# Optimization experiments

Hardware: AMD Instinct MI355X
Metric: run time of the kernel (lower is better)

Reference implementation:

```python
import jax, jax.numpy as jnp
import numpy as np

B, N, D_FEAT = 16, 4096, 64
NPOINT, NSAMPLE = 1024, 32
MLP = [64, 64, 128]
IN_CH = 3 + D_FEAT
EPS = 1e-5  # BatchNorm eps (torch default)


def _fps(xyz, npoint):
    # Farthest point sampling; sequential scan over npoint steps (matches torch loop).
    b, n, _ = xyz.shape
    def step(carry, _):
        distance, farthest = carry  # (B,N) running min dist, (B,) current centroid idx
        centroid = jnp.take_along_axis(xyz, farthest[:, None, None], axis=1)  # (B,1,3)
        d = jnp.sum((xyz - centroid) ** 2, -1)  # (B,N)
        distance = jnp.minimum(distance, d)
        nxt = jnp.argmax(distance, -1).astype(jnp.int32)
        return (distance, nxt), farthest
    init = (jnp.full((b, n), jnp.inf, dtype=xyz.dtype),
            jnp.full((b,), n // 2, dtype=jnp.int32))
    _, centroids = jax.lax.scan(step, init, None, length=npoint)
    return centroids.T  # (B, npoint)


def _gather(pts, idx):
    # pts: (B,N,C); idx: (B,...) int -> (B,...,C)
    return jax.vmap(lambda p, i: p[i])(pts, idx)


def setup_inputs() -> dict:
    key = jax.random.key(0)
    ks = jax.random.split(key, 16)
    inp = {
        'xyz': jax.random.normal(ks[0], (B, N, 3), jnp.float32),
        'points': jax.random.normal(ks[1], (B, N, D_FEAT), jnp.float32),
    }
    last = IN_CH
    for li, oc in enumerate(MLP):
        inp[f'W{li}'] = jax.random.normal(ks[2 + li], (oc, last), jnp.float32) * (1.0 / np.sqrt(last))
        inp[f'b{li}'] = jnp.zeros((oc,), jnp.float32)
        inp[f'g{li}'] = jnp.ones((oc,), jnp.float32)
        inp[f'be{li}'] = jnp.zeros((oc,), jnp.float32)
        last = oc
    C = MLP[-1]; R = C // 8
    inp['aW1'] = jax.random.normal(ks[10], (R, C), jnp.float32) * (1.0 / np.sqrt(C))
    inp['aW2'] = jax.random.normal(ks[11], (C, R), jnp.float32) * (1.0 / np.sqrt(R))
    return inp


def reference(xyz, points, W0, b0, g0, be0, W1, b1, g1, be1, W2, b2, g2, be2, aW1, aW2):
    fps_idx = _fps(xyz, NPOINT)                 # (B,S) int32
    new_xyz = _gather(xyz, fps_idx)             # (B,S,3)
    # squared distances (B,S,N) via matmul expansion (as torch square_distance)
    d = (-2.0 * jnp.einsum('bsc,bnc->bsn', new_xyz, xyz)
         + jnp.sum(new_xyz ** 2, -1)[..., None]
         + jnp.sum(xyz ** 2, -1)[:, None, :])
    _, idx = jax.lax.top_k(-d, NSAMPLE)         # (B,S,k) nearest neighbors
    grouped_xyz = _gather(xyz, idx)             # (B,S,k,3)
    rel = grouped_xyz - new_xyz[:, :, None, :]  # relative coords
    feat = _gather(points, idx)                 # (B,S,k,D)
    g = jnp.concatenate([rel, feat], axis=-1)   # (B,S,k,3+D) channels-last
    # 1x1 conv MLP + BatchNorm (training-mode batch stats) + ReLU
    for (W, b, ga, be) in ((W0, b0, g0, be0), (W1, b1, g1, be1), (W2, b2, g2, be2)):
        g = jnp.einsum('bskc,oc->bsko', g, W) + b
        mu = g.mean(axis=(0, 1, 2))
        var = g.var(axis=(0, 1, 2))
        g = ga * (g - mu) * jax.lax.rsqrt(var + EPS) + be
        g = jax.nn.relu(g)
    new_points = g.max(axis=2)                  # max over nsample -> (B,S,C)
    # channel attention on (B,C,S) == reductions over S here
    avg = new_points.mean(axis=1)               # (B,C)
    mx = new_points.max(axis=1)                 # (B,C)
    def fc(v):
        return jnp.einsum('cr,br->bc', aW2, jax.nn.relu(jnp.einsum('rc,bc->br', aW1, v)))
    scale = jax.nn.sigmoid(fc(avg) + fc(mx))    # (B,C)
    new_points = new_points * scale[:, None, :]
    return new_xyz, new_points, fps_idx
```

## Files before the change

### kernel.cpp

```cpp
#include <hip/hip_runtime.h>
#include <hip/hip_bf16.h>

#define BB 16
#define NN 4096
#define SS 1024
#define KS 32
#define DF 64
#define INC 67
#define C1 64
#define C2 64
#define C3 128
#define ROWS (BB*SS*KS)
#define EPSBN 1e-5f
#define F_INF (__builtin_inff())

typedef __bf16 bf16;
typedef __bf16 bfrag __attribute__((ext_vector_type(8)));
typedef float  ffrag __attribute__((ext_vector_type(4)));
typedef float  f2    __attribute__((ext_vector_type(2)));
typedef unsigned long long u64;

#define OUT_NXYZ 0
#define OUT_NP   49152
#define OUT_FPS  2146304

#define OFF_FPS   0u
#define OFF_NXYZ  65536u
#define OFF_IDX   262144u
#define OFF_STATS 2359296u
#define OFF_ASUM  2555904u
#define OFF_AMAX  2621440u
#define OFF_BNC   2686976u
#define OFF_SCALE 2690048u
#define OFF_NP0   2698240u
#define OFF_YMAX  11086848u
#define OFF_H1    19475456u
#define OFF_H2    86584320u
#define ZERO_BYTES (196608u + 65536u + 65536u)

#define DPP_MAX_STEP(k, ctrl, rmask, bc) { \
  int _lo = __builtin_amdgcn_update_dpp(0, (int)(unsigned)(k), (ctrl), (rmask), 0xf, (bc)); \
  int _hi = __builtin_amdgcn_update_dpp(0, (int)((k)>>32),     (ctrl), (rmask), 0xf, (bc)); \
  u64 _k2 = ((u64)(unsigned)_hi << 32) | (unsigned)_lo; \
  if (_k2 > (k)) (k) = _k2; }

__device__ __forceinline__ u64 dpp_wavemax64(u64 k){
  DPP_MAX_STEP(k, 0x111, 0xf, true)
  DPP_MAX_STEP(k, 0x112, 0xf, true)
  DPP_MAX_STEP(k, 0x114, 0xf, true)
  DPP_MAX_STEP(k, 0x118, 0xf, true)
  DPP_MAX_STEP(k, 0x142, 0xa, false)
  DPP_MAX_STEP(k, 0x143, 0xc, false)
  return k;
}

__global__ __launch_bounds__(256) void fps_kernel(const float* __restrict__ xyz,
                                                  int* __restrict__ fps_i,
                                                  float* __restrict__ nxyz_ws,
                                                  float* __restrict__ out)
{
  #pragma clang fp contract(off)
  __shared__ __align__(16) float4 lc[NN];
  __shared__ int lfps[SS];
  __shared__ u64 slotk[2][4];
  int b = blockIdx.x, t = threadIdx.x;
  const float* xb = xyz + (size_t)b*NN*3;
  for (int p = t; p < NN; p += 256){
    lc[p] = make_float4(xb[p*3], xb[p*3+1], xb[p*3+2], 0.f);
  }
  __syncthreads();
  f2 px2[8], py2[8], pz2[8], pd2[8];
  int p0 = t*16;
  #pragma unroll
  for (int j=0;j<8;++j){
    float4 a = lc[p0+2*j], c = lc[p0+2*j+1];
    px2[j] = (f2){a.x, c.x}; py2[j] = (f2){a.y, c.y}; pz2[j] = (f2){a.z, c.z};
    pd2[j] = (f2){F_INF, F_INF};
  }
  float cx = lc[NN/2].x, cy = lc[NN/2].y, cz = lc[NN/2].z;
  if (t==0) lfps[0]=NN/2;
  int wv = t >> 6, lane = t & 63;
  for (int it=1; it<SS; ++it){
    f2 c2x = (f2){cx,cx}, c2y = (f2){cy,cy}, c2z = (f2){cz,cz};
    float bv=-1.f; int bi=p0;
    #pragma unroll
    for (int j=0;j<8;++j){
      f2 dx = px2[j]-c2x, dy = py2[j]-c2y, dz = pz2[j]-c2z;
      f2 d = (dx*dx + dy*dy) + dz*dz;
      f2 nd = (f2){fminf(pd2[j].x, d.x), fminf(pd2[j].y, d.y)};
      pd2[j]=nd;
      if (nd.x > bv){ bv=nd.x; bi=p0+2*j; }
      if (nd.y > bv){ bv=nd.y; bi=p0+2*j+1; }
    }
    u64 key = ((u64)__float_as_uint(bv) << 32) | (unsigned)(~bi);
    key = dpp_wavemax64(key);
    key = __shfl(key, 63);
    int p = it & 1;
    if (lane == 0) slotk[p][wv] = key;
    __syncthreads();
    u64 k = slotk[p][t & 3];
    DPP_MAX_STEP(k, 0xB1, 0xf, true)
    DPP_MAX_STEP(k, 0x4E, 0xf, true)
    int i = ~(unsigned)k;
    float4 cc = lc[i];
    cx = cc.x; cy = cc.y; cz = cc.z;
    if (t==0) lfps[it]=i;
  }
  __syncthreads();
  for (int s=t; s<SS; s+=256){
    int i = lfps[s];
    fps_i[b*SS+s]=i;
    out[OUT_FPS + b*SS + s] = (float)i;
    float4 cc = lc[i];
    int o3 = (b*SS+s)*3;
    out[OUT_NXYZ+o3]=cc.x; out[OUT_NXYZ+o3+1]=cc.y; out[OUT_NXYZ+o3+2]=cc.z;
    nxyz_ws[o3]=cc.x; nxyz_ws[o3+1]=cc.y; nxyz_ws[o3+2]=cc.z;
  }
}

__global__ __launch_bounds__(64) void knn_kernel(const float* __restrict__ xyz,
                                                 const float* __restrict__ nxyz,
                                                 int* __restrict__ knn)
{
  __shared__ float ld[NN];
  int lane = threadIdx.x;
  int bs = blockIdx.x;
  int b = bs >> 10;
  const float* xb = xyz + (size_t)b*NN*3;
  float sx=nxyz[bs*3], sy=nxyz[bs*3+1], sz=nxyz[bs*3+2];
  float gv[8]; int gi[8];
  float lv = F_INF; int li = 0;
  #pragma unroll
  for (int g=0; g<8; ++g){
    float bgv = F_INF; int bgi = 0;
    #pragma unroll
    for (int jj=0; jj<8; ++jj){
      int p = (g*8+jj)*64 + lane;
      float dx=xb[p*3]-sx, dy=xb[p*3+1]-sy, dz=xb[p*3+2]-sz;
      float d = dx*dx+dy*dy+dz*dz;
      ld[p] = d;
      if (d < bgv){ bgv=d; bgi=p; }
    }
    gv[g]=bgv; gi[g]=bgi;
    if (bgv < lv){ lv=bgv; li=bgi; }
  }
  int kept = 0;
  for (int it=0; it<KS; ++it){
    u64 mk = ~(((u64)__float_as_uint(lv) << 32) | (unsigned)li);
    mk = dpp_wavemax64(mk);
    mk = __shfl(mk, 63);
    int i = (int)(unsigned)(~mk);
    if (lane==it) kept = i;
    if ((i & 63) == lane){
      int j = i >> 6;
      ld[i] = F_INF;
      int g = j >> 3;
      float bgv=F_INF; int bgi=0;
      for (int jj=0;jj<8;++jj){
        int p = (g*8+jj)*64 + lane;
        float d = ld[p];
        if (d<bgv){bgv=d;bgi=p;}
      }
      #pragma unroll
      for (int q=0;q<8;++q){ if (q==g){ gv[q]=bgv; gi[q]=bgi; } }
      lv=F_INF; li=0;
      #pragma unroll
      for (int q=0;q<8;++q){ if (gv[q]<lv){ lv=gv[q]; li=gi[q]; } }
    }
  }
  if (lane < KS) knn[bs*KS + lane] = kept;
}

__global__ __launch_bounds__(256) void conv1_kernel(const float* __restrict__ xyz,
                                                    const float* __restrict__ points,
                                                    const float* __restrict__ W0,
                                                    const float* __restrict__ b0,
                                                    const float* __restrict__ nxyz,
                                                    const int* __restrict__ knn,
                                                    bf16* __restrict__ h1,
                                                    float* __restrict__ stats)
{
  __shared__ __align__(16) bf16 As[64][104];
  __shared__ __align__(16) bf16 Bs[64][104];
  __shared__ float s1[C1], s2[C1];
  int t = threadIdx.x;
  int Rbase = blockIdx.x * 64;
  if (t < C1){ s1[t]=0.f; s2[t]=0.f; }
  {
    int o = t >> 2, q = t & 3;
    const float* wr = W0 + o*INC;
    for (int cc = q*24; cc < q*24+24; ++cc){
      float w;
      if (cc < 64) w = wr[3+cc];
      else if (cc < 67) w = wr[cc-64];
      else w = 0.f;
      Bs[o][cc] = (bf16)w;
    }
  }
  {
    int r = t >> 2, q = t & 3;
    int R = Rbase + r;
    int bs = R >> 5;
    int bIdx = bs >> 10;
    int nI = knn[R];
    const float* pr = points + ((size_t)(bIdx*NN + nI))*DF + q*16;
    float4 f0 = *(const float4*)(pr);
    float4 f1 = *(const float4*)(pr+4);
    float4 f2v = *(const float4*)(pr+8);
    float4 f3 = *(const float4*)(pr+12);
    bf16* ap = &As[r][q*16];
    ap[0]=(bf16)f0.x; ap[1]=(bf16)f0.y; ap[2]=(bf16)f0.z; ap[3]=(bf16)f0.w;
    ap[4]=(bf16)f1.x; ap[5]=(bf16)f1.y; ap[6]=(bf16)f1.z; ap[7]=(bf16)f1.w;
    ap[8]=(bf16)f2v.x; ap[9]=(bf16)f2v.y; ap[10]=(bf16)f2v.z; ap[11]=(bf16)f2v.w;
    ap[12]=(bf16)f3.x; ap[13]=(bf16)f3.y; ap[14]=(bf16)f3.z; ap[15]=(bf16)f3.w;
    if (q==0){
      const float* xr = xyz + ((size_t)(bIdx*NN + nI))*3;
      const float* nr = nxyz + bs*3;
      As[r][64]=(bf16)(xr[0]-nr[0]);
      As[r][65]=(bf16)(xr[1]-nr[1]);
      As[r][66]=(bf16)(xr[2]-nr[2]);
      for (int cc=67; cc<96; ++cc) As[r][cc]=(bf16)0.f;
    }
  }
  __syncthreads();
  int wv = t >> 6, lane = t & 63;
  int row16 = wv * 16;
  int arow = lane & 15, kgrp = lane >> 4;
  ffrag acc[4] = {};
  #pragma unroll
  for (int kc = 0; kc < 3; ++kc){
    bfrag af = *(const bfrag*)&As[row16 + arow][kc*32 + kgrp*8];
    #pragma unroll
    for (int nt = 0; nt < 4; ++nt){
      bfrag bfv = *(const bfrag*)&Bs[nt*16 + arow][kc*32 + kgrp*8];
      acc[nt] = __builtin_amdgcn_mfma_f32_16x16x32_bf16(af, bfv, acc[nt], 0,0,0);
    }
  }
  #pragma unroll
  for (int nt=0; nt<4; ++nt){
    int c = nt*16 + arow;
    float bias = b0[c];
    float ls1=0.f, ls2=0.f;
    #pragma unroll
    for (int r=0;r<4;++r){
      float y = acc[nt][r] + bias;
      int grow = Rbase + row16 + kgrp*4 + r;
      h1[(size_t)grow*C1 + c] = (bf16)y;
      ls1 += y; ls2 += y*y;
    }
    ls1 += __shfl_xor(ls1, 16); ls1 += __shfl_xor(ls1, 32);
    ls2 += __shfl_xor(ls2, 16); ls2 += __shfl_xor(ls2, 32);
    if (kgrp==0){ atomicAdd(&s1[c], ls1); atomicAdd(&s2[c], ls2); }
  }
  __syncthreads();
  if (t < C1){
    float* gp = stats + (blockIdx.x & 63)*256;
    atomicAdd(&gp[t], s1[t]);
    atomicAdd(&gp[128 + t], s2[t]);
  }
}

__global__ void bnfin_kernel(const float* __restrict__ stats, const float* __restrict__ g,
                             const float* __restrict__ be, float* __restrict__ bnc, int C)
{
  int c = threadIdx.x; if (c >= C) return;
  float a1=0.f, a2=0.f;
  for (int q=0;q<64;++q){ a1 += stats[q*256+c]; a2 += stats[q*256+128+c]; }
  float inv = 1.f/(float)ROWS;
  float mu = a1*inv; float var = a2*inv - mu*mu;
  float a = g[c]*rsqrtf(var + EPSBN);
  bnc[c] = a; bnc[128+c] = be[c] - mu*a;
}

__global__ __launch_bounds__(256) void conv2_kernel(const bf16* __restrict__ h1,
                                                    const float* __restrict__ W1,
                                                    const float* __restrict__ b1,
                                                    const float* __restrict__ bnc,
                                                    bf16* __restrict__ h2,
                                                    float* __restrict__ stats)
{
  __shared__ __align__(16) bf16 As[64][72];
  __shared__ __align__(16) bf16 Bs[64][72];
  __shared__ float s1[C2], s2[C2];
  int t = threadIdx.x;
  int Rbase = blockIdx.x * 64;
  if (t < C2){ s1[t]=0.f; s2[t]=0.f; }
  {
    int o = t >> 2, q = t & 3;
    const float* wr = W1 + o*64 + q*16;
    bf16* bp = &Bs[o][q*16];
    #pragma unroll
    for (int v=0; v<4; ++v){
      float4 f = *(const float4*)(wr + v*4);
      bp[v*4+0]=(bf16)f.x; bp[v*4+1]=(bf16)f.y; bp[v*4+2]=(bf16)f.z; bp[v*4+3]=(bf16)f.w;
    }
  }
  {
    int r = t >> 2, q = t & 3;
    int R = Rbase + r;
    const bf16* hr = h1 + (size_t)R*64 + q*16;
    bfrag h0 = *(const bfrag*)hr;
    bfrag h1v = *(const bfrag*)(hr+8);
    #pragma unroll
    for (int j=0;j<8;++j){
      int c=q*16+j;
      As[r][c] = (bf16)fmaxf(fmaf(bnc[c], (float)h0[j], bnc[128+c]), 0.f);
    }
    #pragma unroll
    for (int j=0;j<8;++j){
      int c=q*16+8+j;
      As[r][c] = (bf16)fmaxf(fmaf(bnc[c], (float)h1v[j], bnc[128+c]), 0.f);
    }
  }
  __syncthreads();
  int wv = t >> 6, lane = t & 63;
  int row16 = wv * 16;
  int arow = lane & 15, kgrp = lane >> 4;
  ffrag acc[4] = {};
  #pragma unroll
  for (int kc = 0; kc < 2; ++kc){
    bfrag af = *(const bfrag*)&As[row16 + arow][kc*32 + kgrp*8];
    #pragma unroll
    for (int nt = 0; nt < 4; ++nt){
      bfrag bfv = *(const bfrag*)&Bs[nt*16 + arow][kc*32 + kgrp*8];
      acc[nt] = __builtin_amdgcn_mfma_f32_16x16x32_bf16(af, bfv, acc[nt], 0,0,0);
    }
  }
  #pragma unroll
  for (int nt=0; nt<4; ++nt){
    int c = nt*16 + arow;
    float bias = b1[c];
    float ls1=0.f, ls2=0.f;
    #pragma unroll
    for (int r=0;r<4;++r){
      float y = acc[nt][r] + bias;
      int grow = Rbase + row16 + kgrp*4 + r;
      h2[(size_t)grow*C2 + c] = (bf16)y;
      ls1 += y; ls2 += y*y;
    }
    ls1 += __shfl_xor(ls1, 16); ls1 += __shfl_xor(ls1, 32);
    ls2 += __shfl_xor(ls2, 16); ls2 += __shfl_xor(ls2, 32);
    if (kgrp==0){ atomicAdd(&s1[c], ls1); atomicAdd(&s2[c], ls2); }
  }
  __syncthreads();
  if (t < C2){
    float* gp = stats + (blockIdx.x & 63)*256;
    atomicAdd(&gp[t], s1[t]);
    atomicAdd(&gp[128 + t], s2[t]);
  }
}

__global__ __launch_bounds__(256) void conv3_kernel(const bf16* __restrict__ h2,
                                                    const float* __restrict__ W2,
                                                    const float* __restrict__ b2,
                                                    const float* __restrict__ bnc,
                                                    float* __restrict__ ymax,
                                                    float* __restrict__ stats)
{
  __shared__ __align__(16) bf16 As[64][72];
  __shared__ __align__(16) bf16 Bs[128][72];
  __shared__ float s1[C3], s2[C3];
  __shared__ float wmax[4][C3];
  int t = threadIdx.x;
  int Rbase = blockIdx.x * 64;
  if (t < C3){ s1[t]=0.f; s2[t]=0.f; }
  {
    int o = t >> 1, q = t & 1;
    const float* wr = W2 + o*64 + q*32;
    bf16* bp = &Bs[o][q*32];
    #pragma unroll
    for (int v=0; v<8; ++v){
      float4 f = *(const float4*)(wr + v*4);
      bp[v*4+0]=(bf16)f.x; bp[v*4+1]=(bf16)f.y; bp[v*4+2]=(bf16)f.z; bp[v*4+3]=(bf16)f.w;
    }
  }
  {
    int r = t >> 2, q = t & 3;
    int R = Rbase + r;
    const bf16* hr = h2 + (size_t)R*64 + q*16;
    bfrag h0 = *(const bfrag*)hr;
    bfrag h1v = *(const bfrag*)(hr+8);
    #pragma unroll
    for (int j=0;j<8;++j){
      int c=q*16+j;
      As[r][c] = (bf16)fmaxf(fmaf(bnc[c], (float)h0[j], bnc[128+c]), 0.f);
    }
    #pragma unroll
    for (int j=0;j<8;++j){
      int c=q*16+8+j;
      As[r][c] = (bf16)fmaxf(fmaf(bnc[c], (float)h1v[j], bnc[128+c]), 0.f);
    }
  }
  __syncthreads();
  int wv = t >> 6, lane = t & 63;
  int row16 = wv * 16;
  int arow = lane & 15, kgrp = lane >> 4;
  ffrag acc[8] = {};
  #pragma unroll
  for (int kc = 0; kc < 2; ++kc){
    bfrag af = *(const bfrag*)&As[row16 + arow][kc*32 + kgrp*8];
    #pragma unroll
    for (int nt = 0; nt < 8; ++nt){
      bfrag bfv = *(const bfrag*)&Bs[nt*16 + arow][kc*32 + kgrp*8];
      acc[nt] = __builtin_amdgcn_mfma_f32_16x16x32_bf16(af, bfv, acc[nt], 0,0,0);
    }
  }
  #pragma unroll
  for (int nt=0; nt<8; ++nt){
    int c = nt*16 + arow;
    float bias = b2[c];
    float ls1=0.f, ls2=0.f, mm=-F_INF;
    #pragma unroll
    for (int r=0;r<4;++r){
      float y = acc[nt][r] + bias;
      ls1 += y; ls2 += y*y; mm = fmaxf(mm, y);
    }
    ls1 += __shfl_xor(ls1, 16); ls1 += __shfl_xor(ls1, 32);
    ls2 += __shfl_xor(ls2, 16); ls2 += __shfl_xor(ls2, 32);
    mm = fmaxf(mm, __shfl_xor(mm, 16)); mm = fmaxf(mm, __shfl_xor(mm, 32));
    if (kgrp==0){ atomicAdd(&s1[c], ls1); atomicAdd(&s2[c], ls2); wmax[wv][c]=mm; }
  }
  __syncthreads();
  {
    int half = t >> 7;
    int c = t & 127;
    float m = fmaxf(wmax[half*2][c], wmax[half*2+1][c]);
    ymax[(size_t)(blockIdx.x*2 + half)*C3 + c] = m;
  }
  if (t < C3){
    float* gp = stats + (blockIdx.x & 63)*256;
    atomicAdd(&gp[t], s1[t]);
    atomicAdd(&gp[128 + t], s2[t]);
  }
}

__global__ __launch_bounds__(256) void attreduce_kernel(const float* __restrict__ ymax,
                                                        const float* __restrict__ bnc,
                                                        float* __restrict__ np0,
                                                        float* __restrict__ asum,
                                                        unsigned* __restrict__ amax)
{
  __shared__ float rs[256], rm[256];
  int t = threadIdx.x;
  int b = blockIdx.x >> 3, sg = blockIdx.x & 7;
  int c = t & 127, h = t >> 7;
  float a = bnc[c], bb = bnc[128+c];
  size_t base = ((size_t)(b*1024 + sg*128 + h*64))*128 + c;
  float s = 0.f, m = 0.f;
  #pragma unroll 4
  for (int j=0;j<64;++j){
    float v = fmaxf(fmaf(a, ymax[base + (size_t)j*128], bb), 0.f);
    np0[base + (size_t)j*128] = v;
    s += v; m = fmaxf(m, v);
  }
  rs[t]=s; rm[t]=m;
  __syncthreads();
  if (t < 128){
    float s2 = rs[t] + rs[t+128];
    float m2 = fmaxf(rm[t], rm[t+128]);
    atomicAdd(&asum[b*128+t], s2);
    atomicMax(&amax[b*128+t], __float_as_uint(m2));
  }
}

__global__ __launch_bounds__(256) void attn_kernel(const float* __restrict__ asum,
                                                   const unsigned* __restrict__ amax,
                                                   const float* __restrict__ aW1,
                                                   const float* __restrict__ aW2,
                                                   float* __restrict__ scale)
{
  __shared__ float avg[16][128], mx[16][128], hA[16][16], hM[16][16];
  int t = threadIdx.x;
  for (int i=t; i<2048; i+=256){
    int b=i>>7, c=i&127;
    avg[b][c]=asum[i]*(1.f/1024.f); mx[b][c]=__uint_as_float(amax[i]);
  }
  __syncthreads();
  {
    int b=t>>4, r=t&15;
    float sa=0.f, sm=0.f;
    for (int c=0;c<128;++c){ float w=aW1[r*128+c]; sa+=w*avg[b][c]; sm+=w*mx[b][c]; }
    hA[b][r]=fmaxf(sa,0.f); hM[b][r]=fmaxf(sm,0.f);
  }
  __syncthreads();
  for (int i=t;i<2048;i+=256){
    int b=i>>7,c=i&127;
    float o=0.f;
    for (int r=0;r<16;++r){ o += aW2[c*16+r]*(hA[b][r]+hM[b][r]); }
    scale[i] = 1.f/(1.f+expf(-o));
  }
}

__global__ __launch_bounds__(256) void finout_kernel(const float* __restrict__ np0,
                                                     const float* __restrict__ scale,
                                                     float* __restrict__ out)
{
  int i = blockIdx.x*256 + threadIdx.x;
  int c = i & 127; int b = i >> 17;
  out[OUT_NP + i] = np0[i] * scale[b*128+c];
}

extern "C" void kernel_launch(void* const* d_in, const int* in_sizes, int n_in,
                              void* d_out, int out_size, void* d_ws, size_t ws_size,
                              hipStream_t stream)
{
  const float* xyz    = (const float*)d_in[0];
  const float* points = (const float*)d_in[1];
  const float* W0 = (const float*)d_in[2];
  const float* b0 = (const float*)d_in[3];
  const float* g0 = (const float*)d_in[4];
  const float* be0= (const float*)d_in[5];
  const float* W1 = (const float*)d_in[6];
  const float* b1 = (const float*)d_in[7];
  const float* g1 = (const float*)d_in[8];
  const float* be1= (const float*)d_in[9];
  const float* W2 = (const float*)d_in[10];
  const float* b2 = (const float*)d_in[11];
  const float* g2 = (const float*)d_in[12];
  const float* be2= (const float*)d_in[13];
  const float* aW1= (const float*)d_in[14];
  const float* aW2= (const float*)d_in[15];
  float* out = (float*)d_out;
  char* ws = (char*)d_ws;

  int*      fpsI  = (int*)(ws + OFF_FPS);
  float*    nxyz  = (float*)(ws + OFF_NXYZ);
  int*      knnI  = (int*)(ws + OFF_IDX);
  float*    stats = (float*)(ws + OFF_STATS);
  float*    asum  = (float*)(ws + OFF_ASUM);
  unsigned* amax  = (unsigned*)(ws + OFF_AMAX);
  float*    bnc   = (float*)(ws + OFF_BNC);
  float*    scl   = (float*)(ws + OFF_SCALE);
  float*    np0   = (float*)(ws + OFF_NP0);
  float*    ymax  = (float*)(ws + OFF_YMAX);
  bf16*     h1    = (bf16*)(ws + OFF_H1);
  bf16*     h2    = (bf16*)(ws + OFF_H2);

  hipMemsetAsync(ws + OFF_STATS, 0, ZERO_BYTES, stream);
  fps_kernel<<<BB, 256, 0, stream>>>(xyz, fpsI, nxyz, out);
  knn_kernel<<<BB*SS, 64, 0, stream>>>(xyz, nxyz, knnI);
  conv1_kernel<<<ROWS/64, 256, 0, stream>>>(xyz, points, W0, b0, nxyz, knnI, h1, stats);
  bnfin_kernel<<<1, 128, 0, stream>>>(stats, g0, be0, bnc, C1);
  conv2_kernel<<<ROWS/64, 256, 0, stream>>>(h1, W1, b1, bnc, h2, stats + 64*256);
  bnfin_kernel<<<1, 128, 0, stream>>>(stats + 64*256, g1, be1, bnc + 256, C2);
  conv3_kernel<<<ROWS/64, 256, 0, stream>>>(h2, W2, b2, bnc + 256, ymax, stats + 2*64*256);
  bnfin_kernel<<<1, 128, 0, stream>>>(stats + 2*64*256, g2, be2, bnc + 512, C3);
  attreduce_kernel<<<BB*8, 256, 0, stream>>>(ymax, bnc + 512, np0, asum, amax);
  attn_kernel<<<1, 256, 0, stream>>>(asum, amax, aW1, aW2, scl);
  finout_kernel<<<(BB*SS*C3)/256, 256, 0, stream>>>(np0, scl, out);
}
```

Before: 1.087 ms.

## Widen FPS to 512 threads, SoA coords, readlane broadcast for wave max

The farthest-point-sampling kernel now runs 512 threads per batch with 8 points per thread. This halves the serial per-iteration distance work but adds two more waves to the per-step block barrier and the cross-wave reduction. Coordinates move from float4 AoS to separate x/y/z shared arrays. The lane-63 broadcast after the DPP wave max switches from a shuffle to scalar readlane in both the FPS and KNN kernels, to shorten the latency-bound reduction chain.

```diff
diff --git a/kernel.cpp b/kernel.cpp
--- a/kernel.cpp
+++ b/kernel.cpp
@@ -54,37 +54,42 @@
   return k;
 }
 
-__global__ __launch_bounds__(256) void fps_kernel(const float* __restrict__ xyz,
+__device__ __forceinline__ u64 bcast63(u64 k){
+  unsigned lo = (unsigned)__builtin_amdgcn_readlane((int)(unsigned)k, 63);
+  unsigned hi = (unsigned)__builtin_amdgcn_readlane((int)(k>>32), 63);
+  return ((u64)hi<<32) | lo;
+}
+
+__global__ __launch_bounds__(512) void fps_kernel(const float* __restrict__ xyz,
                                                   int* __restrict__ fps_i,
                                                   float* __restrict__ nxyz_ws,
                                                   float* __restrict__ out)
 {
   #pragma clang fp contract(off)
-  __shared__ __align__(16) float4 lc[NN];
+  __shared__ float lx[NN], ly[NN], lz[NN];
   __shared__ int lfps[SS];
-  __shared__ u64 slotk[2][4];
+  __shared__ u64 slotk[2][8];
   int b = blockIdx.x, t = threadIdx.x;
   const float* xb = xyz + (size_t)b*NN*3;
-  for (int p = t; p < NN; p += 256){
-    lc[p] = make_float4(xb[p*3], xb[p*3+1], xb[p*3+2], 0.f);
-  }
-  __syncthreads();
-  f2 px2[8], py2[8], pz2[8], pd2[8];
-  int p0 = t*16;
-  #pragma unroll
-  for (int j=0;j<8;++j){
-    float4 a = lc[p0+2*j], c = lc[p0+2*j+1];
-    px2[j] = (f2){a.x, c.x}; py2[j] = (f2){a.y, c.y}; pz2[j] = (f2){a.z, c.z};
+  for (int p = t; p < NN; p += 512){ lx[p]=xb[p*3]; ly[p]=xb[p*3+1]; lz[p]=xb[p*3+2]; }
+  __syncthreads();
+  f2 px2[4], py2[4], pz2[4], pd2[4];
+  int p0 = t*8;
+  #pragma unroll
+  for (int j=0;j<4;++j){
+    px2[j] = (f2){lx[p0+2*j], lx[p0+2*j+1]};
+    py2[j] = (f2){ly[p0+2*j], ly[p0+2*j+1]};
+    pz2[j] = (f2){lz[p0+2*j], lz[p0+2*j+1]};
     pd2[j] = (f2){F_INF, F_INF};
   }
-  float cx = lc[NN/2].x, cy = lc[NN/2].y, cz = lc[NN/2].z;
+  float cx = lx[NN/2], cy = ly[NN/2], cz = lz[NN/2];
   if (t==0) lfps[0]=NN/2;
   int wv = t >> 6, lane = t & 63;
   for (int it=1; it<SS; ++it){
     f2 c2x = (f2){cx,cx}, c2y = (f2){cy,cy}, c2z = (f2){cz,cz};
     float bv=-1.f; int bi=p0;
     #pragma unroll
-    for (int j=0;j<8;++j){
+    for (int j=0;j<4;++j){
       f2 dx = px2[j]-c2x, dy = py2[j]-c2y, dz = pz2[j]-c2z;
       f2 d = (dx*dx + dy*dy) + dz*dz;
       f2 nd = (f2){fminf(pd2[j].x, d.x), fminf(pd2[j].y, d.y)};
@@ -94,27 +99,27 @@
     }
     u64 key = ((u64)__float_as_uint(bv) << 32) | (unsigned)(~bi);
     key = dpp_wavemax64(key);
-    key = __shfl(key, 63);
+    key = bcast63(key);
     int p = it & 1;
     if (lane == 0) slotk[p][wv] = key;
     __syncthreads();
-    u64 k = slotk[p][t & 3];
+    u64 k = slotk[p][t & 7];
     DPP_MAX_STEP(k, 0xB1, 0xf, true)
     DPP_MAX_STEP(k, 0x4E, 0xf, true)
+    DPP_MAX_STEP(k, 0x141, 0xf, true)
     int i = ~(unsigned)k;
-    float4 cc = lc[i];
-    cx = cc.x; cy = cc.y; cz = cc.z;
+    cx = lx[i]; cy = ly[i]; cz = lz[i];
     if (t==0) lfps[it]=i;
   }
   __syncthreads();
-  for (int s=t; s<SS; s+=256){
+  for (int s=t; s<SS; s+=512){
     int i = lfps[s];
     fps_i[b*SS+s]=i;
     out[OUT_FPS + b*SS + s] = (float)i;
-    float4 cc = lc[i];
+    float xx=lx[i], yy=ly[i], zz=lz[i];
     int o3 = (b*SS+s)*3;
-    out[OUT_NXYZ+o3]=cc.x; out[OUT_NXYZ+o3+1]=cc.y; out[OUT_NXYZ+o3+2]=cc.z;
-    nxyz_ws[o3]=cc.x; nxyz_ws[o3+1]=cc.y; nxyz_ws[o3+2]=cc.z;
+    out[OUT_NXYZ+o3]=xx; out[OUT_NXYZ+o3+1]=yy; out[OUT_NXYZ+o3+2]=zz;
+    nxyz_ws[o3]=xx; nxyz_ws[o3+1]=yy; nxyz_ws[o3+2]=zz;
   }
 }
 
@@ -148,7 +153,7 @@
   for (int it=0; it<KS; ++it){
     u64 mk = ~(((u64)__float_as_uint(lv) << 32) | (unsigned)li);
     mk = dpp_wavemax64(mk);
-    mk = __shfl(mk, 63);
+    mk = bcast63(mk);
     int i = (int)(unsigned)(~mk);
     if (lane==it) kept = i;
     if ((i & 63) == lane){
@@ -537,7 +542,7 @@
   bf16*     h2    = (bf16*)(ws + OFF_H2);
 
   hipMemsetAsync(ws + OFF_STATS, 0, ZERO_BYTES, stream);
-  fps_kernel<<<BB, 256, 0, stream>>>(xyz, fpsI, nxyz, out);
+  fps_kernel<<<BB, 512, 0, stream>>>(xyz, fpsI, nxyz, out);
   knn_kernel<<<BB*SS, 64, 0, stream>>>(xyz, nxyz, knnI);
   conv1_kernel<<<ROWS/64, 256, 0, stream>>>(xyz, points, W0, b0, nxyz, knnI, h1, stats);
   bnfin_kernel<<<1, 128, 0, stream>>>(stats, g0, be0, bnc, C1);
```

Result: slower. 1.160 ms (+6.7%).
